# Performance work log

Measured on AMD Instinct MI355X. Metric: run time of the kernel, lower is better.

Reference implementation:

```python
import jax, jax.numpy as jnp
import numpy as np

B, C, L, E = 8192, 45, 21, 22  # batch, channels, seq_len, num selected channels (45//2)


def setup_inputs() -> dict:
    key = jax.random.key(0)
    ks = jax.random.split(key, 15)
    f = lambda k, s: jax.random.normal(k, s, dtype=jnp.float32) * 0.1
    return {
        "x": jax.random.normal(ks[0], (B, C, L), dtype=jnp.float32),
        # group_conv: Conv1d(1, 21, kernel=21) -> weight (out=21, k=21), bias (21,)
        "gc_w": f(ks[1], (21, 21)),
        "gc_b": f(ks[2], (21,)),
        # mlp: Linear(45,25) -> Tanh -> Linear(25,45) -> Tanh
        "w1": f(ks[3], (25, 45)), "b1": f(ks[4], (25,)),
        "w2": f(ks[5], (45, 25)), "b2": f(ks[6], (45,)),
        # 22 Self_atten experts; all convs are 1x1 so weights reduce to vectors
        "wq": f(ks[7], (E, 21)), "bq": f(ks[8], (E, 21)),
        "wk": f(ks[9], (E, 21)), "bk": f(ks[10], (E, 21)),
        "wv": f(ks[11], (E, 21)), "bv": f(ks[12], (E, 21)),
        "wo": f(ks[13], (E, 21)), "bo": f(ks[14], (E,)),
    }


def reference(x, gc_w, gc_b, w1, b1, w2, b2, wq, bq, wk, bk, wv, bv, wo, bo):
    # --- gating: per-channel conv (kernel==length -> 1 output position) ---
    # temp[b,i,o] = sum_l gc_w[o,l] * x[b,i,l] + gc_b[o]
    temp = jnp.einsum('bil,ol->bio', x, gc_w) + gc_b            # (B, 45, 21)
    mx = temp.max(axis=-1)                                      # maxpool over 21 conv channels
    av = temp.mean(axis=-1)                                     # avgpool over 21 conv channels
    mlp = lambda h: jnp.tanh(jnp.tanh(h @ w1.T + b1) @ w2.T + b2)
    gate = jax.nn.softmax(mlp(mx) + mlp(av), axis=1)            # (B, 45)

    # --- routing: top-22 channels by batch-mean gate (torch detaches the mean) ---
    mean_gate = jax.lax.stop_gradient(gate).mean(axis=0)        # (45,)
    _, top_idx = jax.lax.top_k(mean_gate, E)
    sel = jnp.sort(top_idx)  # experts assigned in ascending channel order

    # --- batched Self_atten over the 22 selected channels ---
    xs = x[:, sel, :].transpose(1, 0, 2)                        # (E, B, L)
    q = wq[:, None, None, :] * xs[..., None] + bq[:, None, None, :]   # (E,B,L,21)
    k = wk[:, None, :, None] * xs[:, :, None, :] + bk[:, None, :, None]  # (E,B,21,L)
    v = wv[:, None, :, None] * xs[:, :, None, :] + bv[:, None, :, None]  # (E,B,21,L)
    energy = jnp.einsum('eblc,ebcm->eblm', q, k)                # (E,B,L,L)
    attn = jax.nn.softmax(energy, axis=-1)
    out = jnp.einsum('ebcm,eblm->ebcl', v, attn)                # (E,B,21,L)
    y = jnp.einsum('ec,ebcl->ebl', wo, out) + bo[:, None, None] # (E,B,L)

    routed = y.transpose(1, 0, 2) * gate[:, sel][:, :, None]    # (B,E,L)
    A = jnp.zeros_like(x).at[:, sel, :].set(routed)             # non-selected channels -> 0

    A_flat = A.reshape(A.shape[0], C * L)
    G = x.reshape(x.shape[0], C * L) * A_flat
    return G, A_flat
```

## Files before the change

### kernel.cpp

```cpp
#include <hip/hip_runtime.h>
#include <hip/hip_bf16.h>
#include <float.h>
#include <math.h>

#define BATCH   8192
#define NCH     45
#define SEQL    21
#define NEXP    22
#define ROWLEN  945
#define GOFF    7741440

#define K1_BLOCKS 1024
#define K3_BLOCKS 2048

__device__ __forceinline__ float fast_tanh(float v) {
    const float t = __expf(2.f * v);
    return (t - 1.f) / (t + 1.f);
}

__global__ __launch_bounds__(256) void k1_gate(
    const float* __restrict__ x,
    const float* __restrict__ gc_w, const float* __restrict__ gc_b,
    const float* __restrict__ w1,   const float* __restrict__ b1,
    const float* __restrict__ w2,   const float* __restrict__ b2,
    float* __restrict__ gate_out,   float* __restrict__ partialsT)
{
    __shared__ float xsh[8 * ROWLEN];
    __shared__ float buf45a[4][45];
    __shared__ float buf45b[4][45];
    __shared__ float buf25a[4][25];
    __shared__ float buf25b[4][25];
    __shared__ float part[4][45];

    const int tid  = threadIdx.x;
    const int w    = tid >> 6;
    const int lane = tid & 63;
    const int b_base = blockIdx.x * 8;

    {
        const float4* x4 = (const float4*)(x + (size_t)b_base * ROWLEN);
        float4* xsh4 = (float4*)xsh;
        for (int q = tid; q < 1890; q += 256) xsh4[q] = x4[q];
    }
    __syncthreads();

    float acc = 0.f;

    for (int iter = 0; iter < 2; ++iter) {
        const int bb = w * 2 + iter;
        const int b  = b_base + bb;
        float g = 0.f;
        if (lane < NCH) {
            float xr[SEQL];
            const float* xp = &xsh[bb * ROWLEN + lane * SEQL];
            #pragma unroll
            for (int l = 0; l < SEQL; ++l) xr[l] = xp[l];
            float mx = -FLT_MAX, av = 0.f;
            for (int o = 0; o < SEQL; ++o) {
                float t = gc_b[o];
                #pragma unroll
                for (int l = 0; l < SEQL; ++l) t = fmaf(gc_w[o * SEQL + l], xr[l], t);
                mx = fmaxf(mx, t);
                av += t;
            }
            av *= (1.f / 21.f);
            buf45a[w][lane] = mx;
            buf45b[w][lane] = av;
        }
        __syncthreads();
        if (lane < 25) {
            float tm = b1[lane], ta = b1[lane];
            for (int i = 0; i < NCH; ++i) {
                const float wv = w1[lane * NCH + i];
                tm = fmaf(wv, buf45a[w][i], tm);
                ta = fmaf(wv, buf45b[w][i], ta);
            }
            buf25a[w][lane] = fast_tanh(tm);
            buf25b[w][lane] = fast_tanh(ta);
        }
        __syncthreads();
        if (lane < NCH) {
            float tm = b2[lane], ta = b2[lane];
            for (int j = 0; j < 25; ++j) {
                const float wv = w2[lane * 25 + j];
                tm = fmaf(wv, buf25a[w][j], tm);
                ta = fmaf(wv, buf25b[w][j], ta);
            }
            g = __expf(fast_tanh(tm) + fast_tanh(ta));
            buf45a[w][lane] = g;
        }
        __syncthreads();
        if (lane < NCH) {
            float s = 0.f;
            for (int i = 0; i < NCH; ++i) s += buf45a[w][i];
            const float gt = g / s;
            gate_out[(size_t)b * NCH + lane] = gt;
            acc += gt;
        }
        __syncthreads();
    }

    if (lane < NCH) part[w][lane] = acc;
    __syncthreads();
    if (tid < NCH) {
        partialsT[tid * K1_BLOCKS + blockIdx.x] =
            part[0][tid] + part[1][tid] + part[2][tid] + part[3][tid];
    }
}

__global__ __launch_bounds__(256) void k2_reduce(
    const float* __restrict__ partialsT,
    const float* __restrict__ wq, const float* __restrict__ bq,
    const float* __restrict__ wk, const float* __restrict__ bk,
    const float* __restrict__ wv, const float* __restrict__ bv,
    const float* __restrict__ wo, const float* __restrict__ bo,
    float* __restrict__ mg, float* __restrict__ escal)
{
    const int tid = threadIdx.x;
    const int c   = blockIdx.x;

    if (c < NCH) {
        __shared__ float wsum[4];
        const float4 v = ((const float4*)(partialsT + c * K1_BLOCKS))[tid];
        float s = (v.x + v.y) + (v.z + v.w);
        #pragma unroll
        for (int off = 32; off > 0; off >>= 1) s += __shfl_xor(s, off, 64);
        if ((tid & 63) == 0) wsum[tid >> 6] = s;
        __syncthreads();
        if (tid == 0) mg[c] = (wsum[0] + wsum[1]) + (wsum[2] + wsum[3]);
    } else {
        if (tid < NEXP) {
            const int e = tid;
            float A = 0.f, Cc = 0.f, P = 0.f, Q = 0.f;
            for (int i = 0; i < SEQL; ++i) {
                A  = fmaf(wq[e * SEQL + i], wk[e * SEQL + i], A);
                Cc = fmaf(bq[e * SEQL + i], wk[e * SEQL + i], Cc);
                P  = fmaf(wo[e * SEQL + i], wv[e * SEQL + i], P);
                Q  = fmaf(wo[e * SEQL + i], bv[e * SEQL + i], Q);
            }
            Q += bo[e];
            escal[e] = A; escal[22 + e] = Cc; escal[44 + e] = P; escal[66 + e] = Q;
        }
    }
}

__global__ __launch_bounds__(256) void k3_attn(
    const float* __restrict__ x, const float* __restrict__ gate,
    const float* __restrict__ mg, const float* __restrict__ escal,
    float* __restrict__ out)
{
    __shared__ float xsh[4 * ROWLEN];
    __shared__ float ash[4 * ROWLEN];
    __shared__ float smg[64];
    __shared__ float gat[4][NEXP];
    __shared__ float sA[NEXP], sC[NEXP], sP[NEXP], sQ[NEXP];
    __shared__ int   ssel[NEXP];

    const int tid = threadIdx.x;

    if (tid < 64) smg[tid] = (tid < NCH) ? mg[tid] : -FLT_MAX;
    if (tid >= 64 && tid < 64 + NEXP) {
        const int e = tid - 64;
        sA[e] = escal[e];       sC[e] = escal[22 + e];
        sP[e] = escal[44 + e];  sQ[e] = escal[66 + e];
    }

    const int b0 = blockIdx.x * 4;
    {
        const float4* x4 = (const float4*)x + (size_t)blockIdx.x * 945;
        float4* xsh4 = (float4*)xsh;
        float4* ash4 = (float4*)ash;
        const float4 z = make_float4(0.f, 0.f, 0.f, 0.f);
        for (int q = tid; q < 945; q += 256) {
            xsh4[q] = x4[q];
            ash4[q] = z;
        }
    }
    __syncthreads();

    if (tid < 64) {
        const float v = smg[tid];
        int rank = 0;
        #pragma unroll
        for (int i = 0; i < NCH; ++i) {
            const float u = smg[i];
            rank += (u > v || (u == v && i < tid)) ? 1 : 0;
        }
        const bool seld = (tid < NCH) && (rank < NEXP);
        const unsigned long long m = __ballot(seld);
        if (seld) {
            const int e = __popcll(m & ((1ull << tid) - 1ull));
            ssel[e] = tid;
        }
    }
    __syncthreads();

    if (tid < 4 * NEXP) {
        const int bi = tid / NEXP, e = tid - bi * NEXP;
        gat[bi][e] = gate[(size_t)(b0 + bi) * NCH + ssel[e]];
    }
    __syncthreads();

    {
        const int t0 = (tid * 1848) >> 8;
        const int t1 = ((tid + 1) * 1848) >> 8;
        int cur_be = -1;
        float xr[SEQL];
        float Ae = 0.f, Ce = 0.f, Pe = 0.f, Qe = 0.f, ge = 0.f;
        const float* xp = nullptr;
        float* ap = nullptr;

        for (int tsk = t0; tsk < t1; ++tsk) {
            const int be = (tsk * 3121) >> 16;
            if (be != cur_be) {
                cur_be = be;
                const int bi = (be * 2979) >> 16;
                const int e  = be - bi * NEXP;
                xp = &xsh[bi * ROWLEN + ssel[e] * SEQL];
                ap = &ash[bi * ROWLEN + ssel[e] * SEQL];
                #pragma unroll
                for (int m = 0; m < SEQL; ++m) xr[m] = xp[m];
                Ae = sA[e]; Ce = sC[e]; Pe = sP[e]; Qe = sQ[e];
                ge = gat[bi][e];
            }
            const int l = tsk - cur_be * SEQL;
            const float alpha = fmaf(Ae, xp[l], Ce);
            float den = 0.f, num = 0.f;
            #pragma unroll
            for (int m = 0; m < SEQL; ++m) {
                const float wgt = __expf(alpha * xr[m]);
                den += wgt;
                num = fmaf(xr[m], wgt, num);
            }
            ap[l] = fmaf(Pe, num / den, Qe) * ge;
        }
    }
    __syncthreads();

    {
        const float4* xsh4 = (const float4*)xsh;
        const float4* ash4 = (const float4*)ash;
        float4* g4 = (float4*)out + (size_t)blockIdx.x * 945;
        float4* a4 = (float4*)(out + (size_t)GOFF) + (size_t)blockIdx.x * 945;
        for (int q = tid; q < 945; q += 256) {
            const float4 a = ash4[q];
            const float4 xv = xsh4[q];
            g4[q] = make_float4(a.x * xv.x, a.y * xv.y, a.z * xv.z, a.w * xv.w);
            a4[q] = a;
        }
    }
}

extern "C" void kernel_launch(void* const* d_in, const int* in_sizes, int n_in,
                              void* d_out, int out_size, void* d_ws, size_t ws_size,
                              hipStream_t stream)
{
    const float* x    = (const float*)d_in[0];
    const float* gc_w = (const float*)d_in[1];
    const float* gc_b = (const float*)d_in[2];
    const float* w1   = (const float*)d_in[3];
    const float* b1   = (const float*)d_in[4];
    const float* w2   = (const float*)d_in[5];
    const float* b2   = (const float*)d_in[6];
    const float* wq   = (const float*)d_in[7];
    const float* bq   = (const float*)d_in[8];
    const float* wk   = (const float*)d_in[9];
    const float* bk   = (const float*)d_in[10];
    const float* wv   = (const float*)d_in[11];
    const float* bv   = (const float*)d_in[12];
    const float* wo   = (const float*)d_in[13];
    const float* bo   = (const float*)d_in[14];

    float* ws        = (float*)d_ws;
    float* gateBuf   = ws;
    float* partialsT = ws + 368640;
    float* mg        = ws + 414720;
    float* escal     = ws + 414784;
    float* outF      = (float*)d_out;

    k1_gate<<<dim3(K1_BLOCKS), dim3(256), 0, stream>>>(x, gc_w, gc_b, w1, b1, w2, b2,
                                                       gateBuf, partialsT);
    k2_reduce<<<dim3(46), dim3(256), 0, stream>>>(partialsT, wq, bq, wk, bk, wv, bv,
                                                  wo, bo, mg, escal);
    k3_attn<<<dim3(K3_BLOCKS), dim3(256), 0, stream>>>(x, gateBuf, mg, escal, outF);
}
```

Baseline: 156.7 us.

## Fuse gate, reduction and attention into one cooperative kernel with grid syncs

Replaces the three-kernel pipeline with a single cooperative kernel. Each block keeps its 8 batch rows of x and their gate values in shared memory, and two grid-wide syncs separate the partial reduction, the mean-gate/expert-scalar stage and the attention/output stage. This avoids re-reading x and the gate buffer from global memory, along with two extra kernel launches. It also folds log2e into the energy scalars so the softmax can use exp2f. The cost is relying on 1024 co-resident blocks; the old three-kernel path remains as a fallback.

```diff
diff --git a/kernel.cpp b/kernel.cpp
--- a/kernel.cpp
+++ b/kernel.cpp
@@ -1,5 +1,5 @@
 #include <hip/hip_runtime.h>
-#include <hip/hip_bf16.h>
+#include <hip/hip_cooperative_groups.h>
 #include <float.h>
 #include <math.h>
 
@@ -7,15 +7,219 @@
 #define NCH     45
 #define SEQL    21
 #define NEXP    22
+#define NUN     23
 #define ROWLEN  945
 #define GOFF    7741440
-
-#define K1_BLOCKS 1024
+#define GRID    1024
 #define K3_BLOCKS 2048
+#define LOG2E   1.4426950408889634f
+
+namespace cg = cooperative_groups;
 
 __device__ __forceinline__ float fast_tanh(float v) {
     const float t = __expf(2.f * v);
     return (t - 1.f) / (t + 1.f);
+}
+
+__global__ __launch_bounds__(256, 4) void kfused(
+    const float* __restrict__ x,
+    const float* __restrict__ gc_w, const float* __restrict__ gc_b,
+    const float* __restrict__ w1,   const float* __restrict__ b1,
+    const float* __restrict__ w2,   const float* __restrict__ b2,
+    const float* __restrict__ wq,   const float* __restrict__ bq,
+    const float* __restrict__ wk,   const float* __restrict__ bk,
+    const float* __restrict__ wv,   const float* __restrict__ bv,
+    const float* __restrict__ wo,   const float* __restrict__ bo,
+    float* __restrict__ partialsT,  float* __restrict__ mg,
+    float* __restrict__ escal,      float* __restrict__ out)
+{
+    __shared__ float xsh[8 * ROWLEN];
+    __shared__ float buf45a[4][45], buf45b[4][45];
+    __shared__ float buf25a[4][25], buf25b[4][25];
+    __shared__ float part[4][45];
+    __shared__ float gat[8][45];
+    __shared__ float smg[64];
+    __shared__ float sA[NEXP], sC[NEXP], sP[NEXP], sQ[NEXP];
+    __shared__ int   ssel[NEXP], sunsel[NUN];
+    __shared__ float wsum[4];
+
+    const int tid  = threadIdx.x;
+    const int w    = tid >> 6;
+    const int lane = tid & 63;
+    const int b_base = blockIdx.x * 8;
+
+    {
+        const float4* x4 = (const float4*)(x + (size_t)b_base * ROWLEN);
+        float4* xsh4 = (float4*)xsh;
+        for (int q = tid; q < 1890; q += 256) xsh4[q] = x4[q];
+    }
+    __syncthreads();
+
+    float accg = 0.f;
+    for (int iter = 0; iter < 2; ++iter) {
+        const int bb = w * 2 + iter;
+        float g = 0.f;
+        if (lane < NCH) {
+            float xr[SEQL];
+            const float* xp = &xsh[bb * ROWLEN + lane * SEQL];
+            #pragma unroll
+            for (int l = 0; l < SEQL; ++l) xr[l] = xp[l];
+            float mx = -FLT_MAX, av = 0.f;
+            for (int o = 0; o < SEQL; ++o) {
+                float t = gc_b[o];
+                #pragma unroll
+                for (int l = 0; l < SEQL; ++l) t = fmaf(gc_w[o * SEQL + l], xr[l], t);
+                mx = fmaxf(mx, t);
+                av += t;
+            }
+            av *= (1.f / 21.f);
+            buf45a[w][lane] = mx;
+            buf45b[w][lane] = av;
+        }
+        __syncthreads();
+        if (lane < 25) {
+            float tm = b1[lane], ta = b1[lane];
+            for (int i = 0; i < NCH; ++i) {
+                const float wv_ = w1[lane * NCH + i];
+                tm = fmaf(wv_, buf45a[w][i], tm);
+                ta = fmaf(wv_, buf45b[w][i], ta);
+            }
+            buf25a[w][lane] = fast_tanh(tm);
+            buf25b[w][lane] = fast_tanh(ta);
+        }
+        __syncthreads();
+        if (lane < NCH) {
+            float tm = b2[lane], ta = b2[lane];
+            for (int j = 0; j < 25; ++j) {
+                const float wv_ = w2[lane * 25 + j];
+                tm = fmaf(wv_, buf25a[w][j], tm);
+                ta = fmaf(wv_, buf25b[w][j], ta);
+            }
+            g = __expf(fast_tanh(tm) + fast_tanh(ta));
+            buf45a[w][lane] = g;
+        }
+        __syncthreads();
+        if (lane < NCH) {
+            float s = 0.f;
+            for (int i = 0; i < NCH; ++i) s += buf45a[w][i];
+            const float gt = g / s;
+            gat[bb][lane] = gt;
+            accg += gt;
+        }
+        __syncthreads();
+    }
+
+    if (lane < NCH) part[w][lane] = accg;
+    __syncthreads();
+    if (tid < NCH)
+        partialsT[tid * GRID + blockIdx.x] =
+            part[0][tid] + part[1][tid] + part[2][tid] + part[3][tid];
+
+    cg::this_grid().sync();
+
+    if (blockIdx.x < NCH) {
+        const float4 v = ((const float4*)(partialsT + blockIdx.x * GRID))[tid];
+        float s = (v.x + v.y) + (v.z + v.w);
+        #pragma unroll
+        for (int off = 32; off > 0; off >>= 1) s += __shfl_xor(s, off, 64);
+        if ((tid & 63) == 0) wsum[tid >> 6] = s;
+        __syncthreads();
+        if (tid == 0) mg[blockIdx.x] = (wsum[0] + wsum[1]) + (wsum[2] + wsum[3]);
+    } else if (blockIdx.x == NCH) {
+        if (tid < NEXP) {
+            const int e = tid;
+            float A = 0.f, Cc = 0.f, P = 0.f, Q = 0.f;
+            for (int i = 0; i < SEQL; ++i) {
+                A  = fmaf(wq[e * SEQL + i], wk[e * SEQL + i], A);
+                Cc = fmaf(bq[e * SEQL + i], wk[e * SEQL + i], Cc);
+                P  = fmaf(wo[e * SEQL + i], wv[e * SEQL + i], P);
+                Q  = fmaf(wo[e * SEQL + i], bv[e * SEQL + i], Q);
+            }
+            Q += bo[e];
+            escal[e]      = A  * LOG2E;
+            escal[22 + e] = Cc * LOG2E;
+            escal[44 + e] = P;
+            escal[66 + e] = Q;
+        }
+    }
+
+    cg::this_grid().sync();
+
+    if (tid < 64) smg[tid] = (tid < NCH) ? mg[tid] : -FLT_MAX;
+    if (tid >= 64 && tid < 64 + NEXP) {
+        const int e = tid - 64;
+        sA[e] = escal[e];       sC[e] = escal[22 + e];
+        sP[e] = escal[44 + e];  sQ[e] = escal[66 + e];
+    }
+    __syncthreads();
+
+    if (tid < 64) {
+        const float v = smg[tid];
+        int rank = 0;
+        #pragma unroll
+        for (int i = 0; i < NCH; ++i) {
+            const float u = smg[i];
+            rank += (u > v || (u == v && i < tid)) ? 1 : 0;
+        }
+        const bool seld = (tid < NCH) && (rank < NEXP);
+        const unsigned long long m = __ballot(seld);
+        if (seld) ssel[__popcll(m & ((1ull << tid) - 1ull))] = tid;
+        const bool unsl = (tid < NCH) && (rank >= NEXP);
+        const unsigned long long mu = __ballot(unsl);
+        if (unsl) sunsel[__popcll(mu & ((1ull << tid) - 1ull))] = tid;
+    }
+    __syncthreads();
+
+    {
+        const int t0 = (tid * 3696) >> 8;
+        const int t1 = ((tid + 1) * 3696) >> 8;
+        int cur_be = -1;
+        float xr[SEQL];
+        float Ae = 0.f, Ce = 0.f, Pe = 0.f, Qe = 0.f, ge = 0.f;
+        const float* xp = nullptr;
+        int obase = 0;
+
+        for (int tsk = t0; tsk < t1; ++tsk) {
+            const int be = (tsk * 3121) >> 16;
+            if (be != cur_be) {
+                cur_be = be;
+                const int bi = (be * 2979) >> 16;
+                const int e  = be - bi * NEXP;
+                const int ch = ssel[e];
+                xp = &xsh[bi * ROWLEN + ch * SEQL];
+                #pragma unroll
+                for (int m = 0; m < SEQL; ++m) xr[m] = xp[m];
+                Ae = sA[e]; Ce = sC[e]; Pe = sP[e]; Qe = sQ[e];
+                ge = gat[bi][ch];
+                obase = (b_base + bi) * ROWLEN + ch * SEQL;
+            }
+            const int l = tsk - cur_be * SEQL;
+            const float xl  = xp[l];
+            const float al2 = fmaf(Ae, xl, Ce);
+            float den = 0.f, num = 0.f;
+            #pragma unroll
+            for (int m = 0; m < SEQL; ++m) {
+                const float wgt = exp2f(al2 * xr[m]);
+                den += wgt;
+                num = fmaf(xr[m], wgt, num);
+            }
+            const float a = fmaf(Pe, __fdividef(num, den), Qe) * ge;
+            out[obase + l]        = a * xl;
+            out[GOFF + obase + l] = a;
+        }
+    }
+
+    if (tid < 8 * NUN) {
+        const int bi = tid / NUN;
+        const int u  = tid - bi * NUN;
+        const int ch = sunsel[u];
+        const int ob = (b_base + bi) * ROWLEN + ch * SEQL;
+        #pragma unroll
+        for (int l = 0; l < SEQL; ++l) {
+            out[ob + l]        = 0.f;
+            out[GOFF + ob + l] = 0.f;
+        }
+    }
 }
 
 __global__ __launch_bounds__(256) void k1_gate(
@@ -45,7 +249,6 @@
     __syncthreads();
 
     float acc = 0.f;
-
     for (int iter = 0; iter < 2; ++iter) {
         const int bb = w * 2 + iter;
         const int b  = b_base + bb;
@@ -71,9 +274,9 @@
         if (lane < 25) {
             float tm = b1[lane], ta = b1[lane];
             for (int i = 0; i < NCH; ++i) {
-                const float wv = w1[lane * NCH + i];
-                tm = fmaf(wv, buf45a[w][i], tm);
-                ta = fmaf(wv, buf45b[w][i], ta);
+                const float wv_ = w1[lane * NCH + i];
+                tm = fmaf(wv_, buf45a[w][i], tm);
+                ta = fmaf(wv_, buf45b[w][i], ta);
             }
             buf25a[w][lane] = fast_tanh(tm);
             buf25b[w][lane] = fast_tanh(ta);
@@ -82,9 +285,9 @@
         if (lane < NCH) {
             float tm = b2[lane], ta = b2[lane];
             for (int j = 0; j < 25; ++j) {
-                const float wv = w2[lane * 25 + j];
-                tm = fmaf(wv, buf25a[w][j], tm);
-                ta = fmaf(wv, buf25b[w][j], ta);
+                const float wv_ = w2[lane * 25 + j];
+                tm = fmaf(wv_, buf25a[w][j], tm);
+                ta = fmaf(wv_, buf25b[w][j], ta);
             }
             g = __expf(fast_tanh(tm) + fast_tanh(ta));
             buf45a[w][lane] = g;
@@ -102,10 +305,9 @@
 
     if (lane < NCH) part[w][lane] = acc;
     __syncthreads();
-    if (tid < NCH) {
-        partialsT[tid * K1_BLOCKS + blockIdx.x] =
+    if (tid < NCH)
+        partialsT[tid * GRID + blockIdx.x] =
             part[0][tid] + part[1][tid] + part[2][tid] + part[3][tid];
-    }
 }
 
 __global__ __launch_bounds__(256) void k2_reduce(
@@ -121,7 +323,7 @@
 
     if (c < NCH) {
         __shared__ float wsum[4];
-        const float4 v = ((const float4*)(partialsT + c * K1_BLOCKS))[tid];
+        const float4 v = ((const float4*)(partialsT + c * GRID))[tid];
         float s = (v.x + v.y) + (v.z + v.w);
         #pragma unroll
         for (int off = 32; off > 0; off >>= 1) s += __shfl_xor(s, off, 64);
@@ -272,14 +474,35 @@
     const float* bo   = (const float*)d_in[14];
 
     float* ws        = (float*)d_ws;
-    float* gateBuf   = ws;
-    float* partialsT = ws + 368640;
-    float* mg        = ws + 414720;
-    float* escal     = ws + 414784;
+    float* partialsT = ws;
+    float* mg        = ws + 46080;
+    float* escal     = ws + 46144;
+    float* gateBuf   = ws + 46232;
     float* outF      = (float*)d_out;
 
-    k1_gate<<<dim3(K1_BLOCKS), dim3(256), 0, stream>>>(x, gc_w, gc_b, w1, b1, w2, b2,
-                                                       gateBuf, partialsT);
+    static int use_coop = -1;
+    if (use_coop < 0) {
+        int nb = 0;
+        hipError_t e = hipOccupancyMaxActiveBlocksPerMultiprocessor(&nb, kfused, 256, 0);
+        use_coop = (e == hipSuccess && nb >= 4) ? 1 : 0;
+    }
+
+    if (use_coop) {
+        void* args[] = {
+            (void*)&x,  (void*)&gc_w, (void*)&gc_b, (void*)&w1, (void*)&b1,
+            (void*)&w2, (void*)&b2,   (void*)&wq,   (void*)&bq, (void*)&wk,
+            (void*)&bk, (void*)&wv,   (void*)&bv,   (void*)&wo, (void*)&bo,
+            (void*)&partialsT, (void*)&mg, (void*)&escal, (void*)&outF
+        };
+        hipError_t e = hipLaunchCooperativeKernel(reinterpret_cast<void*>(kfused),
+                                                  dim3(GRID), dim3(256),
+                                                  args, 0, stream);
+        if (e == hipSuccess) return;
+        use_coop = 0;
+    }
+
+    k1_gate<<<dim3(GRID), dim3(256), 0, stream>>>(x, gc_w, gc_b, w1, b1, w2, b2,
+                                                  gateBuf, partialsT);
     k2_reduce<<<dim3(46), dim3(256), 0, stream>>>(partialsT, wq, bq, wk, bk, wv, bv,
                                                   wo, bo, mg, escal);
     k3_attn<<<dim3(K3_BLOCKS), dim3(256), 0, stream>>>(x, gateBuf, mg, escal, outF);
```

New measurement: 155.6 us. Within noise of the previous version (-0.7%).

## Fold reduce kernel into gate kernel via atomics and use exp2 in attention

Applied to the files above, without the earlier changes.

Removes the separate k2_reduce launch. Per-block channel partial sums are now accumulated with atomicAdd into a zeroed mean-gate buffer, and block 0 of the gate kernel computes the per-expert scalars. The attention inner loop uses exp2f with LOG2E pre-folded into the scalars, plus a fast divide. This saves a kernel launch and a partials round trip in exchange for a memset, atomic contention, and a non-deterministic summation order that could in rare cases flip the top-k channel selection.

```diff
diff --git a/kernel.cpp b/kernel.cpp
--- a/kernel.cpp
+++ b/kernel.cpp
@@ -1,5 +1,4 @@
 #include <hip/hip_runtime.h>
-#include <hip/hip_bf16.h>
 #include <float.h>
 #include <math.h>
 
@@ -9,9 +8,9 @@
 #define NEXP    22
 #define ROWLEN  945
 #define GOFF    7741440
-
 #define K1_BLOCKS 1024
 #define K3_BLOCKS 2048
+#define LOG2E   1.4426950408889634f
 
 __device__ __forceinline__ float fast_tanh(float v) {
     const float t = __expf(2.f * v);
@@ -23,7 +22,12 @@
     const float* __restrict__ gc_w, const float* __restrict__ gc_b,
     const float* __restrict__ w1,   const float* __restrict__ b1,
     const float* __restrict__ w2,   const float* __restrict__ b2,
-    float* __restrict__ gate_out,   float* __restrict__ partialsT)
+    const float* __restrict__ wq,   const float* __restrict__ bq,
+    const float* __restrict__ wk,   const float* __restrict__ bk,
+    const float* __restrict__ wv,   const float* __restrict__ bv,
+    const float* __restrict__ wo,   const float* __restrict__ bo,
+    float* __restrict__ gate_out,   float* __restrict__ mg,
+    float* __restrict__ escal)
 {
     __shared__ float xsh[8 * ROWLEN];
     __shared__ float buf45a[4][45];
@@ -36,6 +40,22 @@
     const int w    = tid >> 6;
     const int lane = tid & 63;
     const int b_base = blockIdx.x * 8;
+
+    if (blockIdx.x == 0 && tid < NEXP) {
+        const int e = tid;
+        float A = 0.f, Cc = 0.f, P = 0.f, Q = 0.f;
+        for (int i = 0; i < SEQL; ++i) {
+            A  = fmaf(wq[e * SEQL + i], wk[e * SEQL + i], A);
+            Cc = fmaf(bq[e * SEQL + i], wk[e * SEQL + i], Cc);
+            P  = fmaf(wo[e * SEQL + i], wv[e * SEQL + i], P);
+            Q  = fmaf(wo[e * SEQL + i], bv[e * SEQL + i], Q);
+        }
+        Q += bo[e];
+        escal[e]      = A  * LOG2E;
+        escal[22 + e] = Cc * LOG2E;
+        escal[44 + e] = P;
+        escal[66 + e] = Q;
+    }
 
     {
         const float4* x4 = (const float4*)(x + (size_t)b_base * ROWLEN);
@@ -71,9 +91,9 @@
         if (lane < 25) {
             float tm = b1[lane], ta = b1[lane];
             for (int i = 0; i < NCH; ++i) {
-                const float wv = w1[lane * NCH + i];
-                tm = fmaf(wv, buf45a[w][i], tm);
-                ta = fmaf(wv, buf45b[w][i], ta);
+                const float wv_ = w1[lane * NCH + i];
+                tm = fmaf(wv_, buf45a[w][i], tm);
+                ta = fmaf(wv_, buf45b[w][i], ta);
             }
             buf25a[w][lane] = fast_tanh(tm);
             buf25b[w][lane] = fast_tanh(ta);
@@ -82,9 +102,9 @@
         if (lane < NCH) {
             float tm = b2[lane], ta = b2[lane];
             for (int j = 0; j < 25; ++j) {
-                const float wv = w2[lane * 25 + j];
-                tm = fmaf(wv, buf25a[w][j], tm);
-                ta = fmaf(wv, buf25b[w][j], ta);
+                const float wv_ = w2[lane * 25 + j];
+                tm = fmaf(wv_, buf25a[w][j], tm);
+                ta = fmaf(wv_, buf25b[w][j], ta);
             }
             g = __expf(fast_tanh(tm) + fast_tanh(ta));
             buf45a[w][lane] = g;
@@ -103,44 +123,7 @@
     if (lane < NCH) part[w][lane] = acc;
     __syncthreads();
     if (tid < NCH) {
-        partialsT[tid * K1_BLOCKS + blockIdx.x] =
-            part[0][tid] + part[1][tid] + part[2][tid] + part[3][tid];
-    }
-}
-
-__global__ __launch_bounds__(256) void k2_reduce(
-    const float* __restrict__ partialsT,
-    const float* __restrict__ wq, const float* __restrict__ bq,
-    const float* __restrict__ wk, const float* __restrict__ bk,
-    const float* __restrict__ wv, const float* __restrict__ bv,
-    const float* __restrict__ wo, const float* __restrict__ bo,
-    float* __restrict__ mg, float* __restrict__ escal)
-{
-    const int tid = threadIdx.x;
-    const int c   = blockIdx.x;
-
-    if (c < NCH) {
-        __shared__ float wsum[4];
-        const float4 v = ((const float4*)(partialsT + c * K1_BLOCKS))[tid];
-        float s = (v.x + v.y) + (v.z + v.w);
-        #pragma unroll
-        for (int off = 32; off > 0; off >>= 1) s += __shfl_xor(s, off, 64);
-        if ((tid & 63) == 0) wsum[tid >> 6] = s;
-        __syncthreads();
-        if (tid == 0) mg[c] = (wsum[0] + wsum[1]) + (wsum[2] + wsum[3]);
-    } else {
-        if (tid < NEXP) {
-            const int e = tid;
-            float A = 0.f, Cc = 0.f, P = 0.f, Q = 0.f;
-            for (int i = 0; i < SEQL; ++i) {
-                A  = fmaf(wq[e * SEQL + i], wk[e * SEQL + i], A);
-                Cc = fmaf(bq[e * SEQL + i], wk[e * SEQL + i], Cc);
-                P  = fmaf(wo[e * SEQL + i], wv[e * SEQL + i], P);
-                Q  = fmaf(wo[e * SEQL + i], bv[e * SEQL + i], Q);
-            }
-            Q += bo[e];
-            escal[e] = A; escal[22 + e] = Cc; escal[44 + e] = P; escal[66 + e] = Q;
-        }
+        atomicAdd(&mg[tid], part[0][tid] + part[1][tid] + part[2][tid] + part[3][tid]);
     }
 }
 
@@ -224,15 +207,15 @@
                 ge = gat[bi][e];
             }
             const int l = tsk - cur_be * SEQL;
-            const float alpha = fmaf(Ae, xp[l], Ce);
+            const float al2 = fmaf(Ae, xp[l], Ce);
             float den = 0.f, num = 0.f;
             #pragma unroll
             for (int m = 0; m < SEQL; ++m) {
-                const float wgt = __expf(alpha * xr[m]);
+                const float wgt = exp2f(al2 * xr[m]);
                 den += wgt;
                 num = fmaf(xr[m], wgt, num);
             }
-            ap[l] = fmaf(Pe, num / den, Qe) * ge;
+            ap[l] = fmaf(Pe, __fdividef(num, den), Qe) * ge;
         }
     }
     __syncthreads();
@@ -271,16 +254,16 @@
     const float* wo   = (const float*)d_in[13];
     const float* bo   = (const float*)d_in[14];
 
-    float* ws        = (float*)d_ws;
-    float* gateBuf   = ws;
-    float* partialsT = ws + 368640;
-    float* mg        = ws + 414720;
-    float* escal     = ws + 414784;
-    float* outF      = (float*)d_out;
+    float* ws      = (float*)d_ws;
+    float* mg      = ws;
+    float* escal   = ws + 64;
+    float* gateBuf = ws + 192;
+    float* outF    = (float*)d_out;
+
+    hipMemsetAsync(mg, 0, 64 * sizeof(float), stream);
 
     k1_gate<<<dim3(K1_BLOCKS), dim3(256), 0, stream>>>(x, gc_w, gc_b, w1, b1, w2, b2,
-                                                       gateBuf, partialsT);
-    k2_reduce<<<dim3(46), dim3(256), 0, stream>>>(partialsT, wq, bq, wk, bk, wv, bv,
-                                                  wo, bo, mg, escal);
+                                                       wq, bq, wk, bk, wv, bv, wo, bo,
+                                                       gateBuf, mg, escal);
     k3_attn<<<dim3(K3_BLOCKS), dim3(256), 0, stream>>>(x, gateBuf, mg, escal, outF);
 }
```

After: 173.5 us. 1.11x slower.

## Halve per-block batch in gate and attention kernels, use exp2 softmax

Applied to the files above, without the earlier changes.

The gate kernel now handles 4 batch rows per block instead of 8, and the attention kernel handles 2 instead of 4. This doubles the grid sizes to raise occupancy and shrink shared memory per block. The attention scalars are prescaled by log2(e) so the inner softmax can use a native exp2, and the divide uses __fdividef. The reduction kernel now reads twice as many partials, and the global copies switch from float4 to float2, which may reduce memory-access efficiency.

```diff
diff --git a/kernel.cpp b/kernel.cpp
--- a/kernel.cpp
+++ b/kernel.cpp
@@ -1,5 +1,4 @@
 #include <hip/hip_runtime.h>
-#include <hip/hip_bf16.h>
 #include <float.h>
 #include <math.h>
 
@@ -9,13 +8,25 @@
 #define NEXP    22
 #define ROWLEN  945
 #define GOFF    7741440
-
-#define K1_BLOCKS 1024
-#define K3_BLOCKS 2048
+#define K1_BLOCKS 2048
+#define K3_BLOCKS 4096
+#define LOG2E   1.4426950408889634f
 
 __device__ __forceinline__ float fast_tanh(float v) {
     const float t = __expf(2.f * v);
     return (t - 1.f) / (t + 1.f);
+}
+
+__device__ __forceinline__ float fexp2(float v) {
+#if defined(__has_builtin)
+#if __has_builtin(__builtin_amdgcn_exp2f)
+    return __builtin_amdgcn_exp2f(v);
+#else
+    return __expf(v * 0.6931471805599453f);
+#endif
+#else
+    return __expf(v * 0.6931471805599453f);
+#endif
 }
 
 __global__ __launch_bounds__(256) void k1_gate(
@@ -25,86 +36,76 @@
     const float* __restrict__ w2,   const float* __restrict__ b2,
     float* __restrict__ gate_out,   float* __restrict__ partialsT)
 {
-    __shared__ float xsh[8 * ROWLEN];
-    __shared__ float buf45a[4][45];
-    __shared__ float buf45b[4][45];
-    __shared__ float buf25a[4][25];
-    __shared__ float buf25b[4][25];
-    __shared__ float part[4][45];
+    __shared__ float xsh[4 * ROWLEN];
+    __shared__ float b45a[4][45];
+    __shared__ float b45b[4][45];
+    __shared__ float b25a[4][25];
+    __shared__ float b25b[4][25];
 
     const int tid  = threadIdx.x;
     const int w    = tid >> 6;
     const int lane = tid & 63;
-    const int b_base = blockIdx.x * 8;
+    const int b_base = blockIdx.x * 4;
 
     {
         const float4* x4 = (const float4*)(x + (size_t)b_base * ROWLEN);
         float4* xsh4 = (float4*)xsh;
-        for (int q = tid; q < 1890; q += 256) xsh4[q] = x4[q];
-    }
-    __syncthreads();
-
-    float acc = 0.f;
-
-    for (int iter = 0; iter < 2; ++iter) {
-        const int bb = w * 2 + iter;
-        const int b  = b_base + bb;
-        float g = 0.f;
-        if (lane < NCH) {
-            float xr[SEQL];
-            const float* xp = &xsh[bb * ROWLEN + lane * SEQL];
+        for (int q = tid; q < 945; q += 256) xsh4[q] = x4[q];
+    }
+    __syncthreads();
+
+    float g = 0.f;
+    if (lane < NCH) {
+        float xr[SEQL];
+        const float* xp = &xsh[w * ROWLEN + lane * SEQL];
+        #pragma unroll
+        for (int l = 0; l < SEQL; ++l) xr[l] = xp[l];
+        float mx = -FLT_MAX, av = 0.f;
+        for (int o = 0; o < SEQL; ++o) {
+            float t = gc_b[o];
             #pragma unroll
-            for (int l = 0; l < SEQL; ++l) xr[l] = xp[l];
-            float mx = -FLT_MAX, av = 0.f;
-            for (int o = 0; o < SEQL; ++o) {
-                float t = gc_b[o];
-                #pragma unroll
-                for (int l = 0; l < SEQL; ++l) t = fmaf(gc_w[o * SEQL + l], xr[l], t);
-                mx = fmaxf(mx, t);
-                av += t;
-            }
-            av *= (1.f / 21.f);
-            buf45a[w][lane] = mx;
-            buf45b[w][lane] = av;
-        }
-        __syncthreads();
-        if (lane < 25) {
-            float tm = b1[lane], ta = b1[lane];
-            for (int i = 0; i < NCH; ++i) {
-                const float wv = w1[lane * NCH + i];
-                tm = fmaf(wv, buf45a[w][i], tm);
-                ta = fmaf(wv, buf45b[w][i], ta);
-            }
-            buf25a[w][lane] = fast_tanh(tm);
-            buf25b[w][lane] = fast_tanh(ta);
-        }
-        __syncthreads();
-        if (lane < NCH) {
-            float tm = b2[lane], ta = b2[lane];
-            for (int j = 0; j < 25; ++j) {
-                const float wv = w2[lane * 25 + j];
-                tm = fmaf(wv, buf25a[w][j], tm);
-                ta = fmaf(wv, buf25b[w][j], ta);
-            }
-            g = __expf(fast_tanh(tm) + fast_tanh(ta));
-            buf45a[w][lane] = g;
-        }
-        __syncthreads();
-        if (lane < NCH) {
-            float s = 0.f;
-            for (int i = 0; i < NCH; ++i) s += buf45a[w][i];
-            const float gt = g / s;
-            gate_out[(size_t)b * NCH + lane] = gt;
-            acc += gt;
-        }
-        __syncthreads();
-    }
-
-    if (lane < NCH) part[w][lane] = acc;
+            for (int l = 0; l < SEQL; ++l) t = fmaf(gc_w[o * SEQL + l], xr[l], t);
+            mx = fmaxf(mx, t);
+            av += t;
+        }
+        av *= (1.f / 21.f);
+        b45a[w][lane] = mx;
+        b45b[w][lane] = av;
+    }
+    __syncthreads();
+    if (lane < 25) {
+        float tm = b1[lane], ta = b1[lane];
+        for (int i = 0; i < NCH; ++i) {
+            const float wv_ = w1[lane * NCH + i];
+            tm = fmaf(wv_, b45a[w][i], tm);
+            ta = fmaf(wv_, b45b[w][i], ta);
+        }
+        b25a[w][lane] = fast_tanh(tm);
+        b25b[w][lane] = fast_tanh(ta);
+    }
+    __syncthreads();
+    if (lane < NCH) {
+        float tm = b2[lane], ta = b2[lane];
+        for (int j = 0; j < 25; ++j) {
+            const float wv_ = w2[lane * 25 + j];
+            tm = fmaf(wv_, b25a[w][j], tm);
+            ta = fmaf(wv_, b25b[w][j], ta);
+        }
+        g = __expf(fast_tanh(tm) + fast_tanh(ta));
+        b45a[w][lane] = g;
+    }
+    __syncthreads();
+    if (lane < NCH) {
+        float s = 0.f;
+        for (int i = 0; i < NCH; ++i) s += b45a[w][i];
+        const float gt = g / s;
+        gate_out[(size_t)(b_base + w) * NCH + lane] = gt;
+        b45b[w][lane] = gt;
+    }
     __syncthreads();
     if (tid < NCH) {
         partialsT[tid * K1_BLOCKS + blockIdx.x] =
-            part[0][tid] + part[1][tid] + part[2][tid] + part[3][tid];
+            b45b[0][tid] + b45b[1][tid] + b45b[2][tid] + b45b[3][tid];
     }
 }
 
@@ -121,8 +122,10 @@
 
     if (c < NCH) {
         __shared__ float wsum[4];
-        const float4 v = ((const float4*)(partialsT + c * K1_BLOCKS))[tid];
-        float s = (v.x + v.y) + (v.z + v.w);
+        const float4* p4 = (const float4*)(partialsT + c * K1_BLOCKS);
+        const float4 v0 = p4[tid];
+        const float4 v1 = p4[tid + 256];
+        float s = ((v0.x + v0.y) + (v0.z + v0.w)) + ((v1.x + v1.y) + (v1.z + v1.w));
         #pragma unroll
         for (int off = 32; off > 0; off >>= 1) s += __shfl_xor(s, off, 64);
         if ((tid & 63) == 0) wsum[tid >> 6] = s;
@@ -139,7 +142,10 @@
                 Q  = fmaf(wo[e * SEQL + i], bv[e * SEQL + i], Q);
             }
             Q += bo[e];
-            escal[e] = A; escal[22 + e] = Cc; escal[44 + e] = P; escal[66 + e] = Q;
+            escal[e]      = A  * LOG2E;
+            escal[22 + e] = Cc * LOG2E;
+            escal[44 + e] = P;
+            escal[66 + e] = Q;
         }
     }
 }
@@ -149,10 +155,10 @@
     const float* __restrict__ mg, const float* __restrict__ escal,
     float* __restrict__ out)
 {
-    __shared__ float xsh[4 * ROWLEN];
-    __shared__ float ash[4 * ROWLEN];
+    __shared__ float xsh[2 * ROWLEN];
+    __shared__ float ash[2 * ROWLEN];
     __shared__ float smg[64];
-    __shared__ float gat[4][NEXP];
+    __shared__ float gat[2][NEXP];
     __shared__ float sA[NEXP], sC[NEXP], sP[NEXP], sQ[NEXP];
     __shared__ int   ssel[NEXP];
 
@@ -165,15 +171,15 @@
         sP[e] = escal[44 + e];  sQ[e] = escal[66 + e];
     }
 
-    const int b0 = blockIdx.x * 4;
-    {
-        const float4* x4 = (const float4*)x + (size_t)blockIdx.x * 945;
-        float4* xsh4 = (float4*)xsh;
-        float4* ash4 = (float4*)ash;
-        const float4 z = make_float4(0.f, 0.f, 0.f, 0.f);
+    const int b0 = blockIdx.x * 2;
+    {
+        const float2* x2 = (const float2*)(x + (size_t)b0 * ROWLEN);
+        float2* xsh2 = (float2*)xsh;
+        float2* ash2 = (float2*)ash;
+        const float2 z = make_float2(0.f, 0.f);
         for (int q = tid; q < 945; q += 256) {
-            xsh4[q] = x4[q];
-            ash4[q] = z;
+            xsh2[q] = x2[q];
+            ash2[q] = z;
         }
     }
     __syncthreads();
@@ -195,15 +201,16 @@
     }
     __syncthreads();
 
-    if (tid < 4 * NEXP) {
-        const int bi = tid / NEXP, e = tid - bi * NEXP;
+    if (tid < 2 * NEXP) {
+        const int bi = (tid >= NEXP) ? 1 : 0;
+        const int e  = tid - bi * NEXP;
         gat[bi][e] = gate[(size_t)(b0 + bi) * NCH + ssel[e]];
     }
     __syncthreads();
 
     {
-        const int t0 = (tid * 1848) >> 8;
-        const int t1 = ((tid + 1) * 1848) >> 8;
+        const int t0 = (tid * 924) >> 8;
+        const int t1 = ((tid + 1) * 924) >> 8;
         int cur_be = -1;
         float xr[SEQL];
         float Ae = 0.f, Ce = 0.f, Pe = 0.f, Qe = 0.f, ge = 0.f;
@@ -224,29 +231,29 @@
                 ge = gat[bi][e];
             }
             const int l = tsk - cur_be * SEQL;
-            const float alpha = fmaf(Ae, xp[l], Ce);
+            const float al2 = fmaf(Ae, xp[l], Ce);
             float den = 0.f, num = 0.f;
             #pragma unroll
             for (int m = 0; m < SEQL; ++m) {
-                const float wgt = __expf(alpha * xr[m]);
+                const float wgt = fexp2(al2 * xr[m]);
                 den += wgt;
                 num = fmaf(xr[m], wgt, num);
             }
-            ap[l] = fmaf(Pe, num / den, Qe) * ge;
-        }
-    }
-    __syncthreads();
-
-    {
-        const float4* xsh4 = (const float4*)xsh;
-        const float4* ash4 = (const float4*)ash;
-        float4* g4 = (float4*)out + (size_t)blockIdx.x * 945;
-        float4* a4 = (float4*)(out + (size_t)GOFF) + (size_t)blockIdx.x * 945;
+            ap[l] = fmaf(Pe, __fdividef(num, den), Qe) * ge;
+        }
+    }
+    __syncthreads();
+
+    {
+        const float2* xsh2 = (const float2*)xsh;
+        const float2* ash2 = (const float2*)ash;
+        float2* g2 = (float2*)out + (size_t)blockIdx.x * 945;
+        float2* a2 = (float2*)(out + (size_t)GOFF) + (size_t)blockIdx.x * 945;
         for (int q = tid; q < 945; q += 256) {
-            const float4 a = ash4[q];
-            const float4 xv = xsh4[q];
-            g4[q] = make_float4(a.x * xv.x, a.y * xv.y, a.z * xv.z, a.w * xv.w);
-            a4[q] = a;
+            const float2 a = ash2[q];
+            const float2 xv = xsh2[q];
+            g2[q] = make_float2(a.x * xv.x, a.y * xv.y);
+            a2[q] = a;
         }
     }
 }
@@ -272,10 +279,10 @@
     const float* bo   = (const float*)d_in[14];
 
     float* ws        = (float*)d_ws;
-    float* gateBuf   = ws;
-    float* partialsT = ws + 368640;
-    float* mg        = ws + 414720;
-    float* escal     = ws + 414784;
+    float* partialsT = ws;
+    float* mg        = ws + 92160;
+    float* escal     = ws + 92224;
+    float* gateBuf   = ws + 92352;
     float* outF      = (float*)d_out;
 
     k1_gate<<<dim3(K1_BLOCKS), dim3(256), 0, stream>>>(x, gc_w, gc_b, w1, b1, w2, b2,
```

Result: faster. 151.5 us (-3.3%).
